# Optimization experiments

Hardware: AMD Instinct MI355X
Metric: run time of the kernel (lower is better)

Reference implementation:

```python
import jax, jax.numpy as jnp
import numpy as np
import math

NUM_HEADS = 16
HIDDEN = 1024
HEAD_DIM = HIDDEN // NUM_HEADS
WIN = 512  # relative position window size
B, S = 2, 2048
LN_EPS = 1e-5


def setup_inputs() -> dict:
    key = jax.random.key(0)
    ks = jax.random.split(key, 8)
    sd = 1.0 / math.sqrt(HIDDEN)
    return {
        "x": jax.random.normal(ks[0], (B, S, HIDDEN), jnp.float32),
        "Wq": jax.random.normal(ks[1], (HIDDEN, HIDDEN), jnp.float32) * sd,
        "bq": jnp.zeros((HIDDEN,), jnp.float32),
        "Wk": jax.random.normal(ks[2], (HIDDEN, HIDDEN), jnp.float32) * sd,
        "bk": jnp.zeros((HIDDEN,), jnp.float32),
        "Wv": jax.random.normal(ks[3], (HIDDEN, HIDDEN), jnp.float32) * sd,
        "bv": jnp.zeros((HIDDEN,), jnp.float32),
        "Wo": jax.random.normal(ks[4], (HIDDEN, HIDDEN), jnp.float32) * sd,
        "bo": jnp.zeros((HIDDEN,), jnp.float32),
        "relpos_table": jax.random.normal(ks[5], (WIN, HIDDEN), jnp.float32),
        "ln_gamma": jnp.ones((HIDDEN,), jnp.float32),
        "ln_beta": jnp.zeros((HIDDEN,), jnp.float32),
        "Wrk": jax.random.normal(ks[6], (HIDDEN, HIDDEN), jnp.float32) * sd,
        "brk": jnp.zeros((HIDDEN,), jnp.float32),
        "Wrq": jax.random.normal(ks[7], (HIDDEN, HIDDEN), jnp.float32) * sd,
        "brq": jnp.zeros((HIDDEN,), jnp.float32),
    }


def reference(x, Wq, bq, Wk, bk, Wv, bv, Wo, bo,
              relpos_table, ln_gamma, ln_beta, Wrk, brk, Wrq, brq):
    Bsz, Slen, H = x.shape
    nh, hd = NUM_HEADS, HEAD_DIM

    # QKV projections -> [B, S, nh, hd]
    q = (x @ Wq + bq).reshape(Bsz, Slen, nh, hd)
    k = (x @ Wk + bk).reshape(Bsz, Slen, nh, hd)
    v = (x @ Wv + bv).reshape(Bsz, Slen, nh, hd)

    mu = relpos_table.mean(-1, keepdims=True)
    var = relpos_table.var(-1, keepdims=True)  # biased, as in torch LayerNorm
    e = (relpos_table - mu) * jax.lax.rsqrt(var + LN_EPS) * ln_gamma + ln_beta

    # relative position index matrix [S, S]: clamp(key - query, -W+1, 0) + W-1
    qi = jnp.arange(Slen)
    relpos = jnp.clip(qi[None, :] - qi[:, None], -WIN + 1, 0) + (WIN - 1)

    rk = (e @ Wrk + brk).reshape(WIN, nh, hd)
    rq = (e @ Wrq + brq).reshape(WIN, nh, hd)

    # content-to-content scores [B, nh, S, S]
    c2c = jnp.einsum('bqhd,bkhd->bhqk', q, k)

    # content-to-position: scores over window then gather along window axis
    qps = jnp.einsum('bnhd,whd->bhnw', q, rk)           # [B, nh, S, W]
    c2p = qps[:, :, qi[:, None], relpos]                # [B, nh, S, S]

    # position-to-content: window x key_seq scores, gather along window axis
    kps = jnp.einsum('bnhd,whd->bhwn', k, rq)           # [B, nh, W, S]
    p2c = kps[:, :, relpos, qi[None, :]]                # [B, nh, S, S]

    scale_factor = 3.0  # 1 + relpos_q_enabled + relpos_k_enabled
    logits = (c2c + c2p + p2c) / math.sqrt(hd * scale_factor)

    # causal mask
    causal = qi[None, :] <= qi[:, None]
    logits = jnp.where(causal[None, None], logits, jnp.finfo(logits.dtype).min)

    attn = jax.nn.softmax(logits, axis=-1)              # [B, nh, S, S]
    out = jnp.einsum('bhqk,bkhd->bqhd', attn, v).reshape(Bsz, Slen, H)
    return out @ Wo + bo
```

## Files before the change

kernel.cpp:

```cpp
#include <hip/hip_runtime.h>
#include <math.h>

#define NH 16
#define HD 64
#define HID 1024
#define SEQ 2048
#define NB 2

typedef __attribute__((ext_vector_type(8))) short short8;
typedef __attribute__((ext_vector_type(4))) float f32x4;
typedef unsigned short u16;
typedef unsigned int u32;

constexpr float LN_EPS_C = 1e-5f;
constexpr float SM_SCALE = 0.07216878364870323f;

__device__ inline u16 f2b(float f) {
  unsigned u = __builtin_bit_cast(unsigned, f);
  u = (u + 0x7FFFu + ((u >> 16) & 1u)) >> 16;
  return (u16)u;
}
__device__ inline float b2f(u16 h) {
  unsigned u = ((unsigned)h) << 16;
  return __builtin_bit_cast(float, u);
}
__device__ inline u32 pk2(float lo, float hi) {
  return (u32)f2b(lo) | ((u32)f2b(hi) << 16);
}
__device__ inline f32x4 mfma16(short8 a, short8 b, f32x4 c) {
  return __builtin_amdgcn_mfma_f32_16x16x32_bf16(a, b, c, 0, 0, 0);
}
__device__ inline short8 swz8(const u16* base, int row, int hc) {
  return *reinterpret_cast<const short8*>(&base[row * 64 + 8 * (hc ^ (row & 7))]);
}
__device__ inline int vrot(int row, int col) {
  return row * 72 + ((col + 16 * ((row >> 3) & 3)) & 63);
}
template <int N>
__device__ inline float rorf(float x) {
  return __builtin_bit_cast(float,
      __builtin_amdgcn_update_dpp(0, __builtin_bit_cast(int, x),
                                  0x120 + N, 0xF, 0xF, true));
}
__device__ inline float rmax16(float x) {
  x = fmaxf(x, rorf<1>(x)); x = fmaxf(x, rorf<2>(x));
  x = fmaxf(x, rorf<4>(x)); x = fmaxf(x, rorf<8>(x));
  return x;
}
__device__ inline float rsum16(float x) {
  x += rorf<1>(x); x += rorf<2>(x); x += rorf<4>(x); x += rorf<8>(x);
  return x;
}

struct PrepArgs {
  const float* tbl; const float* gamma; const float* beta; u16* e;
  const float* x; u16* xb;
  const float* ws[6]; u16* wd[6];
};
__global__ __launch_bounds__(256) void prep_kernel(PrepArgs p) {
  __shared__ float T[32][33];
  __shared__ float sb[4], ssb[4];
  int bid = blockIdx.x;
  int t = threadIdx.x;
  if (bid < 512) {
    int row = bid;
    const float4* rp = reinterpret_cast<const float4*>(p.tbl + (size_t)row * HID);
    float4 x = rp[t];
    float s = x.x + x.y + x.z + x.w;
    float ss = x.x * x.x + x.y * x.y + x.z * x.z + x.w * x.w;
    #pragma unroll
    for (int o = 1; o < 64; o <<= 1) {
      s += __shfl_xor(s, o);
      ss += __shfl_xor(ss, o);
    }
    int w = t >> 6;
    if ((t & 63) == 0) { sb[w] = s; ssb[w] = ss; }
    __syncthreads();
    s = sb[0] + sb[1] + sb[2] + sb[3];
    ss = ssb[0] + ssb[1] + ssb[2] + ssb[3];
    float mu = s * (1.0f / HID);
    float var = ss * (1.0f / HID) - mu * mu;
    float rs = rsqrtf(var + LN_EPS_C);
    float4 g = reinterpret_cast<const float4*>(p.gamma)[t];
    float4 bt = reinterpret_cast<const float4*>(p.beta)[t];
    ushort4 o4;
    o4.x = f2b((x.x - mu) * rs * g.x + bt.x);
    o4.y = f2b((x.y - mu) * rs * g.y + bt.y);
    o4.z = f2b((x.z - mu) * rs * g.z + bt.z);
    o4.w = f2b((x.w - mu) * rs * g.w + bt.w);
    *reinterpret_cast<ushort4*>(&p.e[(size_t)row * HID + t * 4]) = o4;
  } else if (bid < 2560) {
    int i = ((bid - 512) * 256 + t) * 8;
    float4 a = *reinterpret_cast<const float4*>(&p.x[i]);
    float4 c = *reinterpret_cast<const float4*>(&p.x[i + 4]);
    short8 o;
    o[0] = (short)f2b(a.x); o[1] = (short)f2b(a.y); o[2] = (short)f2b(a.z); o[3] = (short)f2b(a.w);
    o[4] = (short)f2b(c.x); o[5] = (short)f2b(c.y); o[6] = (short)f2b(c.z); o[7] = (short)f2b(c.w);
    *reinterpret_cast<short8*>(&p.xb[i]) = o;
  } else {
    int z = (bid - 2560) >> 10;
    int rem = (bid - 2560) & 1023;
    int bn = (rem & 31) * 32, bk = (rem >> 5) * 32;
    const float* W = p.ws[z];
    u16* Wt = p.wd[z];
    int r = t >> 3, c4 = (t & 7) * 4;
    float4 v = *reinterpret_cast<const float4*>(&W[(size_t)(bk + r) * HID + bn + c4]);
    T[r][c4 + 0] = v.x; T[r][c4 + 1] = v.y; T[r][c4 + 2] = v.z; T[r][c4 + 3] = v.w;
    __syncthreads();
    int n = t >> 3, k4 = (t & 7) * 4;
    ushort4 o;
    o.x = f2b(T[k4 + 0][n]); o.y = f2b(T[k4 + 1][n]);
    o.z = f2b(T[k4 + 2][n]); o.w = f2b(T[k4 + 3][n]);
    *reinterpret_cast<ushort4*>(&Wt[(size_t)(bn + n) * HID + bk + k4]) = o;
  }
}

struct GO {
  const float* bias[3];
  void* out[3];
};
template <bool F32OUT>
__global__ __launch_bounds__(512) void gemm_bf16(const u16* __restrict__ A,
    const u16* __restrict__ Bt, GO go) {
  __shared__ u16 Al[8192];
  __shared__ u16 Bl[8192];
  int t = threadIdx.x;
  int gx = gridDim.x;
  int nwg = gx * gridDim.y;
  int lin = blockIdx.y * gx + blockIdx.x;
  lin = (lin & 7) * (nwg >> 3) + (lin >> 3);
  int cb = (lin % gx) * 128, rb = (lin / gx) * 128;
  int which = cb >> 10, cbl = cb & 1023;
  const float* bias = go.bias[which];
  void* Cout = go.out[which];
  int wv = t >> 6, lane = t & 63, l15 = lane & 15, lg = lane >> 4;
  int wr = (wv >> 2) * 64, wc = (wv & 3) * 32;
  int srow = t >> 2, sch = t & 3;
  f32x4 acc[4][2];
  #pragma unroll
  for (int i = 0; i < 4; ++i)
    #pragma unroll
    for (int j = 0; j < 2; ++j) acc[i][j] = (f32x4){0.f, 0.f, 0.f, 0.f};
  const u16* Ap = A + (size_t)(rb + srow) * HID;
  const u16* Bp = Bt + (size_t)(cb + srow) * HID;
  int slot0 = 8 * (sch ^ (srow & 7));
  int slot1 = 8 * ((sch + 4) ^ (srow & 7));
  short8 pa0 = *reinterpret_cast<const short8*>(&Ap[sch * 8]);
  short8 pa1 = *reinterpret_cast<const short8*>(&Ap[(sch + 4) * 8]);
  short8 pb0 = *reinterpret_cast<const short8*>(&Bp[sch * 8]);
  short8 pb1 = *reinterpret_cast<const short8*>(&Bp[(sch + 4) * 8]);
  for (int kk = 0; kk < HID; kk += 64) {
    __syncthreads();
    *reinterpret_cast<short8*>(&Al[srow * 64 + slot0]) = pa0;
    *reinterpret_cast<short8*>(&Al[srow * 64 + slot1]) = pa1;
    *reinterpret_cast<short8*>(&Bl[srow * 64 + slot0]) = pb0;
    *reinterpret_cast<short8*>(&Bl[srow * 64 + slot1]) = pb1;
    __syncthreads();
    if (kk + 64 < HID) {
      pa0 = *reinterpret_cast<const short8*>(&Ap[kk + 64 + sch * 8]);
      pa1 = *reinterpret_cast<const short8*>(&Ap[kk + 64 + (sch + 4) * 8]);
      pb0 = *reinterpret_cast<const short8*>(&Bp[kk + 64 + sch * 8]);
      pb1 = *reinterpret_cast<const short8*>(&Bp[kk + 64 + (sch + 4) * 8]);
    }
    #pragma unroll
    for (int s = 0; s < 2; ++s) {
      short8 am[4], bn[2];
      #pragma unroll
      for (int i = 0; i < 4; ++i) am[i] = swz8(Al, wr + i * 16 + l15, s * 4 + lg);
      #pragma unroll
      for (int j = 0; j < 2; ++j) bn[j] = swz8(Bl, wc + j * 16 + l15, s * 4 + lg);
      #pragma unroll
      for (int i = 0; i < 4; ++i)
        #pragma unroll
        for (int j = 0; j < 2; ++j)
          acc[i][j] = mfma16(am[i], bn[j], acc[i][j]);
    }
  }
  #pragma unroll
  for (int j = 0; j < 2; ++j) {
    float bv = bias[cbl + wc + j * 16 + l15];
    #pragma unroll
    for (int i = 0; i < 4; ++i) {
      #pragma unroll
      for (int r = 0; r < 4; ++r) {
        size_t idx = (size_t)(rb + wr + i * 16 + lg * 4 + r) * HID + cbl + wc + j * 16 + l15;
        float v = acc[i][j][r] + bv;
        if (F32OUT) reinterpret_cast<float*>(Cout)[idx] = v;
        else reinterpret_cast<u16*>(Cout)[idx] = f2b(v);
      }
    }
  }
}

template <bool F32OUT>
__global__ __launch_bounds__(256) void gemm_m64(const u16* __restrict__ A,
    const u16* __restrict__ Bt, GO go) {
  __shared__ u16 Al[4096];
  __shared__ u16 Bl[8192];
  int t = threadIdx.x;
  int gx = gridDim.x;
  int nwg = gx * gridDim.y;
  int lin = blockIdx.y * gx + blockIdx.x;
  lin = (lin & 7) * (nwg >> 3) + (lin >> 3);
  int cb = (lin % gx) * 128, rb = (lin / gx) * 64;
  int which = cb >> 10, cbl = cb & 1023;
  const float* bias = go.bias[which];
  void* Cout = go.out[which];
  int wv = t >> 6, lane = t & 63, l15 = lane & 15, lg = lane >> 4;
  int wc = wv * 32;
  int arow = t >> 2, ach = t & 3;
  int aslot0 = 8 * (ach ^ (arow & 7));
  int aslot1 = 8 * ((ach + 4) ^ (arow & 7));
  int brow = t >> 1, bch = (t & 1) * 4;
  const u16* Ap = A + (size_t)(rb + arow) * HID;
  const u16* Bp = Bt + (size_t)(cb + brow) * HID;
  f32x4 acc[4][2];
  #pragma unroll
  for (int i = 0; i < 4; ++i)
    #pragma unroll
    for (int j = 0; j < 2; ++j) acc[i][j] = (f32x4){0.f, 0.f, 0.f, 0.f};
  short8 pa0 = *reinterpret_cast<const short8*>(&Ap[ach * 8]);
  short8 pa1 = *reinterpret_cast<const short8*>(&Ap[(ach + 4) * 8]);
  short8 pb[4];
  #pragma unroll
  for (int j = 0; j < 4; ++j)
    pb[j] = *reinterpret_cast<const short8*>(&Bp[(bch + j) * 8]);
  for (int kk = 0; kk < HID; kk += 64) {
    __syncthreads();
    *reinterpret_cast<short8*>(&Al[arow * 64 + aslot0]) = pa0;
    *reinterpret_cast<short8*>(&Al[arow * 64 + aslot1]) = pa1;
    #pragma unroll
    for (int j = 0; j < 4; ++j)
      *reinterpret_cast<short8*>(&Bl[brow * 64 + 8 * ((bch + j) ^ (brow & 7))]) = pb[j];
    __syncthreads();
    if (kk + 64 < HID) {
      pa0 = *reinterpret_cast<const short8*>(&Ap[kk + 64 + ach * 8]);
      pa1 = *reinterpret_cast<const short8*>(&Ap[kk + 64 + (ach + 4) * 8]);
      #pragma unroll
      for (int j = 0; j < 4; ++j)
        pb[j] = *reinterpret_cast<const short8*>(&Bp[kk + 64 + (bch + j) * 8]);
    }
    #pragma unroll
    for (int s = 0; s < 2; ++s) {
      short8 am[4], bn[2];
      #pragma unroll
      for (int i = 0; i < 4; ++i) am[i] = swz8(Al, i * 16 + l15, s * 4 + lg);
      #pragma unroll
      for (int j = 0; j < 2; ++j) bn[j] = swz8(Bl, wc + j * 16 + l15, s * 4 + lg);
      #pragma unroll
      for (int i = 0; i < 4; ++i)
        #pragma unroll
        for (int j = 0; j < 2; ++j)
          acc[i][j] = mfma16(am[i], bn[j], acc[i][j]);
    }
  }
  #pragma unroll
  for (int j = 0; j < 2; ++j) {
    float bv = bias[cbl + wc + j * 16 + l15];
    #pragma unroll
    for (int i = 0; i < 4; ++i) {
      #pragma unroll
      for (int r = 0; r < 4; ++r) {
        size_t idx = (size_t)(rb + i * 16 + lg * 4 + r) * HID + cbl + wc + j * 16 + l15;
        float v = acc[i][j][r] + bv;
        if (F32OUT) reinterpret_cast<float*>(Cout)[idx] = v;
        else reinterpret_cast<u16*>(Cout)[idx] = f2b(v);
      }
    }
  }
}

__global__ __launch_bounds__(256, 3) void bias_kernel(
    const u16* __restrict__ Qb, const u16* __restrict__ Kb,
    const u16* __restrict__ RKb, const u16* __restrict__ RQb,
    u16* __restrict__ bandT, float* __restrict__ qrk0,
    float* __restrict__ krq0) {
  __shared__ u16 smem[20992];
  const int KsO = 0, UO = 4096;
  const int RKO = UO, RQO = UO + 8192;
  const int G1O = UO, G2O = UO + 8448;

  int qt = blockIdx.x;
  int h = blockIdx.y, b = blockIdx.z;
  int q0 = qt * 64;
  int t = threadIdx.x;
  int wv = t >> 6, lane = t & 63, l15 = lane & 15, lg = lane >> 4;
  int qs = q0 + wv * 16;
  int hoff = h * HD;
  int bh = (b * NH + h) * SEQ;

  {
    int i = q0 + (t >> 2);
    int sub = t & 3;
    size_t rbase = (size_t)(b * SEQ + i) * HID + hoff + sub * 16;
    size_t tb2 = (size_t)hoff + sub * 16;
    float s1 = 0.f, s2 = 0.f;
    #pragma unroll
    for (int c = 0; c < 2; ++c) {
      short8 qv = *reinterpret_cast<const short8*>(&Qb[rbase + c * 8]);
      short8 rv = *reinterpret_cast<const short8*>(&RKb[tb2 + c * 8]);
      short8 kv = *reinterpret_cast<const short8*>(&Kb[rbase + c * 8]);
      short8 uv = *reinterpret_cast<const short8*>(&RQb[tb2 + c * 8]);
      #pragma unroll
      for (int j = 0; j < 8; ++j) {
        s1 += b2f((u16)qv[j]) * b2f((u16)rv[j]);
        s2 += b2f((u16)kv[j]) * b2f((u16)uv[j]);
      }
    }
    s1 += __shfl_xor(s1, 1); s1 += __shfl_xor(s1, 2);
    s2 += __shfl_xor(s2, 1); s2 += __shfl_xor(s2, 2);
    if (sub == 0) { qrk0[bh + i] = s1 * SM_SCALE; krq0[bh + i] = s2 * SM_SCALE; }
  }

  size_t qgrow = (size_t)(b * SEQ + qs + l15) * HID + hoff;
  short8 aq0 = *reinterpret_cast<const short8*>(&Qb[qgrow + lg * 8]);
  short8 aq1 = *reinterpret_cast<const short8*>(&Qb[qgrow + 32 + lg * 8]);

  const f32x4 Z = (f32x4){0.f, 0.f, 0.f, 0.f};
  int vr = t >> 2, vc8 = (t & 3) * 8;
  int ktlo = qt - 8; if (ktlo < 0) ktlo = 0;
  size_t tbase = (((size_t)(b * NH + h) * 32 + qt) * 9) << 12;

  for (int kt = ktlo; kt <= qt; ++kt) {
    int k0 = kt * 64;
    int dt = qt - kt;
    int wlo = 448 - 64 * dt; if (wlo < 0) wlo = 0;
    __syncthreads();
    {
      const u16* kg = &Kb[(size_t)(b * SEQ + k0 + vr) * HID + hoff];
      int c0 = vc8 >> 3;
      *reinterpret_cast<short8*>(&smem[KsO + vr * 64 + 8 * (c0 ^ (vr & 7))]) =
          *reinterpret_cast<const short8*>(&kg[vc8]);
      *reinterpret_cast<short8*>(&smem[KsO + vr * 64 + 8 * ((c0 + 4) ^ (vr & 7))]) =
          *reinterpret_cast<const short8*>(&kg[vc8 + 32]);
    }
    for (int e2 = t; e2 < 1024; e2 += 256) {
      int rr = e2 >> 3, cch = e2 & 7;
      int wr2 = wlo + rr; if (wr2 > 511) wr2 = 511;
      size_t gb = (size_t)wr2 * HID + hoff + cch * 8;
      int slot = 8 * (cch ^ (rr & 7));
      *reinterpret_cast<short8*>(&smem[RKO + rr * 64 + slot]) =
          *reinterpret_cast<const short8*>(&RKb[gb]);
      *reinterpret_cast<short8*>(&smem[RQO + rr * 64 + slot]) =
          *reinterpret_cast<const short8*>(&RQb[gb]);
    }
    __syncthreads();
    u32 g1p[16], g2p[16];
    #pragma unroll
    for (int cw = 0; cw < 8; ++cw) {
      short8 r0 = swz8(&smem[RKO], cw * 16 + l15, lg);
      short8 r1 = swz8(&smem[RKO], cw * 16 + l15, 4 + lg);
      f32x4 g = mfma16(r1, aq1, mfma16(r0, aq0, Z));
      g1p[2 * cw] = pk2(g[0], g[1]);
      g1p[2 * cw + 1] = pk2(g[2], g[3]);
    }
    short8 kw0 = swz8(&smem[KsO], wv * 16 + l15, lg);
    short8 kw1 = swz8(&smem[KsO], wv * 16 + l15, 4 + lg);
    #pragma unroll
    for (int cw = 0; cw < 8; ++cw) {
      short8 u0 = swz8(&smem[RQO], cw * 16 + l15, lg);
      short8 u1 = swz8(&smem[RQO], cw * 16 + l15, 4 + lg);
      f32x4 g = mfma16(u1, kw1, mfma16(u0, kw0, Z));
      g2p[2 * cw] = pk2(g[0], g[1]);
      g2p[2 * cw + 1] = pk2(g[2], g[3]);
    }
    __syncthreads();
    #pragma unroll
    for (int cw = 0; cw < 8; ++cw) {
      *reinterpret_cast<uint2*>(&smem[G1O + (wv * 16 + l15) * 132 + cw * 16 + lg * 4]) =
          make_uint2(g1p[2 * cw], g1p[2 * cw + 1]);
      *reinterpret_cast<uint2*>(&smem[G2O + (wv * 16 + l15) * 132 + cw * 16 + lg * 4]) =
          make_uint2(g2p[2 * cw], g2p[2 * cw + 1]);
    }
    __syncthreads();
    u16* outp = bandT + tbase + ((size_t)dt << 12) + t * 16;
    #pragma unroll
    for (int c = 0; c < 4; ++c) {
      float vv[4];
      #pragma unroll
      for (int r = 0; r < 4; ++r) {
        int q = qs + lg * 4 + r;
        int k = k0 + c * 16 + l15;
        int wi = 511 - (q - k) - wlo; if (wi < 0) wi = 0;
        vv[r] = (b2f(smem[G1O + (wv * 16 + lg * 4 + r) * 132 + wi]) +
                 b2f(smem[G2O + (c * 16 + l15) * 132 + wi])) * SM_SCALE;
      }
      *reinterpret_cast<uint2*>(outp + c * 4) =
          make_uint2(pk2(vv[0], vv[1]), pk2(vv[2], vv[3]));
    }
  }
}

__global__ __launch_bounds__(256, 2) void attn_mfma(
    const u16* __restrict__ Qb, const u16* __restrict__ Kb,
    const u16* __restrict__ Vb, const float* __restrict__ qrk0,
    const float* __restrict__ krq0, const u16* __restrict__ bandT,
    u16* __restrict__ ATT) {
  __shared__ u16 smem[22016];
  const int KsB[2] = {0, 4096};
  const int VtB[2] = {8192, 12800};
  const int PsO = 17408;

  int qtA = 31 - (int)blockIdx.x;
  int qtB = (int)blockIdx.x;
  int h = blockIdx.y, b = blockIdx.z;
  int t = threadIdx.x;
  int wv = t >> 6, lane = t & 63, l15 = lane & 15, lg = lane >> 4;
  int hoff = h * HD;
  int bh = (b * NH + h) * SEQ;
  size_t tbaseA = (((size_t)(b * NH + h) * 32 + qtA) * 9) << 12;
  size_t tbaseB = (((size_t)(b * NH + h) * 32 + qtB) * 9) << 12;

  int qsA = qtA * 64 + wv * 16;
  int qsB = qtB * 64 + wv * 16;
  size_t qgA = (size_t)(b * SEQ + qsA + l15) * HID + hoff;
  size_t qgB = (size_t)(b * SEQ + qsB + l15) * HID + hoff;
  short8 aqA0 = *reinterpret_cast<const short8*>(&Qb[qgA + lg * 8]);
  short8 aqA1 = *reinterpret_cast<const short8*>(&Qb[qgA + 32 + lg * 8]);
  short8 aqB0 = *reinterpret_cast<const short8*>(&Qb[qgB + lg * 8]);
  short8 aqB1 = *reinterpret_cast<const short8*>(&Qb[qgB + 32 + lg * 8]);
  float qb0A[4], qb0B[4];
  #pragma unroll
  for (int r = 0; r < 4; ++r) {
    qb0A[r] = qrk0[bh + qsA + lg * 4 + r];
    qb0B[r] = qrk0[bh + qsB + lg * 4 + r];
  }

  float mA[4], lA[4], mB[4], lB[4];
  f32x4 oA[4], oB[4];
  #pragma unroll
  for (int r = 0; r < 4; ++r) { mA[r] = -INFINITY; lA[r] = 0.f; mB[r] = -INFINITY; lB[r] = 0.f; }
  #pragma unroll
  for (int c = 0; c < 4; ++c) {
    oA[c] = (f32x4){0.f, 0.f, 0.f, 0.f};
    oB[c] = (f32x4){0.f, 0.f, 0.f, 0.f};
  }

  const f32x4 Z = (f32x4){0.f, 0.f, 0.f, 0.f};
  int vr = t >> 2, vc8 = (t & 3) * 8;
  int c0s = vc8 >> 3;
  int kslot0 = vr * 64 + 8 * (c0s ^ (vr & 7));
  int kslot1 = vr * 64 + 8 * ((c0s + 4) ^ (vr & 7));
  int vslot[16];
  #pragma unroll
  for (int j = 0; j < 8; ++j) {
    vslot[j] = vrot(vc8 + j, vr);
    vslot[8 + j] = vrot(vc8 + 32 + j, vr);
  }

  {
    const u16* kg = &Kb[(size_t)(b * SEQ + vr) * HID + hoff];
    short8 k0v = *reinterpret_cast<const short8*>(&kg[vc8]);
    short8 k1v = *reinterpret_cast<const short8*>(&kg[vc8 + 32]);
    *reinterpret_cast<short8*>(&smem[KsB[0] + kslot0]) = k0v;
    *reinterpret_cast<short8*>(&smem[KsB[0] + kslot1]) = k1v;
    const u16* vg = &Vb[(size_t)(b * SEQ + vr) * HID + hoff];
    short8 v0v = *reinterpret_cast<const short8*>(&vg[vc8]);
    short8 v1v = *reinterpret_cast<const short8*>(&vg[vc8 + 32]);
    #pragma unroll
    for (int j = 0; j < 8; ++j) smem[VtB[0] + vslot[j]] = (u16)v0v[j];
    #pragma unroll
    for (int j = 0; j < 8; ++j) smem[VtB[0] + vslot[8 + j]] = (u16)v1v[j];
  }
  __syncthreads();

  int cur = 0;
  for (int kt = 0; kt <= qtA; ++kt) {
    int k0 = kt * 64;
    int dtA = qtA - kt;
    bool doB = (kt <= qtB);
    int dtB = qtB - kt;
    bool bandedA = (dtA <= 8);
    bool bandedB = doB && (dtB <= 8);
    int ksb = KsB[cur], vtb = VtB[cur];
    int ksn = KsB[cur ^ 1], vtn = VtB[cur ^ 1];

    short8 pA0, pA1, pB0, pB1;
    if (bandedA) {
      const u16* tb = bandT + tbaseA + ((size_t)dtA << 12) + t * 16;
      pA0 = *reinterpret_cast<const short8*>(tb);
      pA1 = *reinterpret_cast<const short8*>(tb + 8);
    }
    if (bandedB) {
      const u16* tb = bandT + tbaseB + ((size_t)dtB << 12) + t * 16;
      pB0 = *reinterpret_cast<const short8*>(tb);
      pB1 = *reinterpret_cast<const short8*>(tb + 8);
    }
    float kq[4];
    if (dtA > 8 || (doB && dtB > 8)) {
      #pragma unroll
      for (int c = 0; c < 4; ++c) kq[c] = krq0[bh + k0 + c * 16 + l15];
    }
    short8 nk0, nk1, nv0, nv1;
    if (kt < qtA) {
      const u16* kg = &Kb[(size_t)(b * SEQ + k0 + 64 + vr) * HID + hoff];
      nk0 = *reinterpret_cast<const short8*>(&kg[vc8]);
      nk1 = *reinterpret_cast<const short8*>(&kg[vc8 + 32]);
      const u16* vg = &Vb[(size_t)(b * SEQ + k0 + 64 + vr) * HID + hoff];
      nv0 = *reinterpret_cast<const short8*>(&vg[vc8]);
      nv1 = *reinterpret_cast<const short8*>(&vg[vc8 + 32]);
    }

    short8 kb0[4], kb1[4];
    #pragma unroll
    for (int c = 0; c < 4; ++c) {
      kb0[c] = swz8(&smem[ksb], c * 16 + l15, lg);
      kb1[c] = swz8(&smem[ksb], c * 16 + l15, 4 + lg);
    }
    f32x4 sA[4], sB[4];
    __builtin_amdgcn_s_setprio(1);
    #pragma unroll
    for (int c = 0; c < 4; ++c)
      sA[c] = mfma16(aqA1, kb1[c], mfma16(aqA0, kb0[c], Z));
    if (doB) {
      #pragma unroll
      for (int c = 0; c < 4; ++c)
        sB[c] = mfma16(aqB1, kb1[c], mfma16(aqB0, kb0[c], Z));
    }
    __builtin_amdgcn_s_setprio(0);
    #pragma unroll
    for (int c = 0; c < 4; ++c) {
      #pragma unroll
      for (int r = 0; r < 4; ++r) {
        float bbv = bandedA ? b2f((u16)((c < 2 ? pA0 : pA1)[(c & 1) * 4 + r]))
                            : qb0A[r] + kq[c];
        float v = fmaf(sA[c][r], SM_SCALE, bbv);
        if (dtA == 0) {
          int ql = wv * 16 + lg * 4 + r, kl = c * 16 + l15;
          if (ql < kl) v = -INFINITY;
        }
        sA[c][r] = v;
      }
    }
    if (doB) {
      #pragma unroll
      for (int c = 0; c < 4; ++c) {
        #pragma unroll
        for (int r = 0; r < 4; ++r) {
          float bbv = bandedB ? b2f((u16)((c < 2 ? pB0 : pB1)[(c & 1) * 4 + r]))
                              : qb0B[r] + kq[c];
          float v = fmaf(sB[c][r], SM_SCALE, bbv);
          if (dtB == 0) {
            int ql = wv * 16 + lg * 4 + r, kl = c * 16 + l15;
            if (ql < kl) v = -INFINITY;
          }
          sB[c][r] = v;
        }
      }
    }
    float alA[4], alB[4];
    #pragma unroll
    for (int r = 0; r < 4; ++r) {
      float mx = fmaxf(fmaxf(sA[0][r], sA[1][r]), fmaxf(sA[2][r], sA[3][r]));
      mx = rmax16(mx);
      float mn = fmaxf(mA[r], mx);
      alA[r] = __expf(mA[r] - mn);
      float ps = 0.f;
      #pragma unroll
      for (int c = 0; c < 4; ++c) {
        float p = __expf(sA[c][r] - mn);
        sA[c][r] = p;
        ps += p;
      }
      ps = rsum16(ps);
      lA[r] = lA[r] * alA[r] + ps;
      mA[r] = mn;
    }
    if (doB) {
      #pragma unroll
      for (int r = 0; r < 4; ++r) {
        float mx = fmaxf(fmaxf(sB[0][r], sB[1][r]), fmaxf(sB[2][r], sB[3][r]));
        mx = rmax16(mx);
        float mn = fmaxf(mB[r], mx);
        alB[r] = __expf(mB[r] - mn);
        float ps = 0.f;
        #pragma unroll
        for (int c = 0; c < 4; ++c) {
          float p = __expf(sB[c][r] - mn);
          sB[c][r] = p;
          ps += p;
        }
        ps = rsum16(ps);
        lB[r] = lB[r] * alB[r] + ps;
        mB[r] = mn;
      }
    }
    short8 vb0[4], vb1[4];
    #pragma unroll
    for (int c = 0; c < 4; ++c) {
      int n = c * 16 + l15;
      vb0[c] = *reinterpret_cast<const short8*>(&smem[vtb + vrot(n, lg * 8)]);
      vb1[c] = *reinterpret_cast<const short8*>(&smem[vtb + vrot(n, 32 + lg * 8)]);
    }
    #pragma unroll
    for (int c = 0; c < 4; ++c) {
      #pragma unroll
      for (int r = 0; r < 4; ++r) {
        smem[PsO + vrot(wv * 16 + lg * 4 + r, c * 16 + l15)] = f2b(sA[c][r]);
        oA[c][r] *= alA[r];
      }
    }
    int prow = wv * 16 + l15;
    {
      short8 ap0 = *reinterpret_cast<const short8*>(&smem[PsO + vrot(prow, lg * 8)]);
      short8 ap1 = *reinterpret_cast<const short8*>(&smem[PsO + vrot(prow, 32 + lg * 8)]);
      __builtin_amdgcn_s_setprio(1);
      #pragma unroll
      for (int c = 0; c < 4; ++c)
        oA[c] = mfma16(ap1, vb1[c], mfma16(ap0, vb0[c], oA[c]));
      __builtin_amdgcn_s_setprio(0);
    }
    if (doB) {
      #pragma unroll
      for (int c = 0; c < 4; ++c) {
        #pragma unroll
        for (int r = 0; r < 4; ++r) {
          smem[PsO + vrot(wv * 16 + lg * 4 + r, c * 16 + l15)] = f2b(sB[c][r]);
          oB[c][r] *= alB[r];
        }
      }
      short8 bp0 = *reinterpret_cast<const short8*>(&smem[PsO + vrot(prow, lg * 8)]);
      short8 bp1 = *reinterpret_cast<const short8*>(&smem[PsO + vrot(prow, 32 + lg * 8)]);
      __builtin_amdgcn_s_setprio(1);
      #pragma unroll
      for (int c = 0; c < 4; ++c)
        oB[c] = mfma16(bp1, vb1[c], mfma16(bp0, vb0[c], oB[c]));
      __builtin_amdgcn_s_setprio(0);
    }
    if (kt < qtA) {
      *reinterpret_cast<short8*>(&smem[ksn + kslot0]) = nk0;
      *reinterpret_cast<short8*>(&smem[ksn + kslot1]) = nk1;
      #pragma unroll
      for (int j = 0; j < 8; ++j) smem[vtn + vslot[j]] = (u16)nv0[j];
      #pragma unroll
      for (int j = 0; j < 8; ++j) smem[vtn + vslot[8 + j]] = (u16)nv1[j];
    }
    __syncthreads();
    cur ^= 1;
  }
  #pragma unroll
  for (int r = 0; r < 4; ++r) { lA[r] = 1.0f / lA[r]; lB[r] = 1.0f / lB[r]; }
  #pragma unroll
  for (int c = 0; c < 4; ++c) {
    #pragma unroll
    for (int r = 0; r < 4; ++r) {
      size_t obA = (size_t)(b * SEQ + qsA + lg * 4 + r) * HID + hoff + c * 16 + l15;
      ATT[obA] = f2b(oA[c][r] * lA[r]);
      size_t obB = (size_t)(b * SEQ + qsB + lg * 4 + r) * HID + hoff + c * 16 + l15;
      ATT[obB] = f2b(oB[c][r] * lB[r]);
    }
  }
}

extern "C" void kernel_launch(void* const* d_in, const int* in_sizes, int n_in,
                              void* d_out, int out_size, void* d_ws, size_t ws_size,
                              hipStream_t stream) {
  const float* x      = (const float*)d_in[0];
  const float* Wq     = (const float*)d_in[1];
  const float* bq     = (const float*)d_in[2];
  const float* Wk     = (const float*)d_in[3];
  const float* bk     = (const float*)d_in[4];
  const float* Wv     = (const float*)d_in[5];
  const float* bv     = (const float*)d_in[6];
  const float* Wo     = (const float*)d_in[7];
  const float* bo     = (const float*)d_in[8];
  const float* relpos = (const float*)d_in[9];
  const float* gamma  = (const float*)d_in[10];
  const float* beta   = (const float*)d_in[11];
  const float* Wrk    = (const float*)d_in[12];
  const float* brk    = (const float*)d_in[13];
  const float* Wrq    = (const float*)d_in[14];
  const float* brq    = (const float*)d_in[15];
  float* out = (float*)d_out;

  u16* wsu = (u16*)d_ws;
  size_t off = 0;
  auto alloc = [&](size_t n) { u16* p = wsu + off; off += n; return p; };
  u16* xb   = alloc(4194304);
  u16* Eb   = alloc(524288);
  u16* WtQ  = alloc(1048576);
  u16* WtK  = alloc(1048576);
  u16* WtV  = alloc(1048576);
  u16* WtO  = alloc(1048576);
  u16* WtRK = alloc(1048576);
  u16* WtRQ = alloc(1048576);
  u16* Qb2  = alloc(4194304);
  u16* Kb2  = alloc(4194304);
  u16* Vb2  = alloc(4194304);
  u16* ATTb = alloc(4194304);
  u16* RKb2 = alloc(524288);
  u16* RQb2 = alloc(524288);
  float* qrk0 = (float*)(wsu + off); off += 131072;
  float* krq0 = (float*)(wsu + off); off += 131072;
  u16* bandT = alloc((size_t)NB * NH * 32 * 9 * 4096);

  PrepArgs pa;
  pa.tbl = relpos; pa.gamma = gamma; pa.beta = beta; pa.e = Eb;
  pa.x = x; pa.xb = xb;
  pa.ws[0] = Wq; pa.ws[1] = Wk; pa.ws[2] = Wv; pa.ws[3] = Wo; pa.ws[4] = Wrk; pa.ws[5] = Wrq;
  pa.wd[0] = WtQ; pa.wd[1] = WtK; pa.wd[2] = WtV; pa.wd[3] = WtO; pa.wd[4] = WtRK; pa.wd[5] = WtRQ;
  prep_kernel<<<8704, 256, 0, stream>>>(pa);

  GO goQKV = {{bq, bk, bv}, {Qb2, Kb2, Vb2}};
  dim3 gQKV(24, 32);
  gemm_bf16<false><<<gQKV, 512, 0, stream>>>(xb, WtQ, goQKV);
  GO goRel = {{brk, brq, brq}, {RKb2, RQb2, RQb2}};
  dim3 gRel2(16, 8);
  gemm_m64<false><<<gRel2, 256, 0, stream>>>(Eb, WtRK, goRel);

  dim3 gB(32, NH, NB);
  bias_kernel<<<gB, 256, 0, stream>>>(Qb2, Kb2, RKb2, RQb2, bandT, qrk0, krq0);

  dim3 gA(16, NH, NB);
  attn_mfma<<<gA, 256, 0, stream>>>(Qb2, Kb2, Vb2, qrk0, krq0, bandT, ATTb);

  GO goOut = {{bo, bo, bo}, {out, out, out}};
  dim3 gOut(8, 64);
  gemm_m64<true><<<gOut, 256, 0, stream>>>(ATTb, WtO, goOut);
}
```

Baseline: 210.7 us.

## Merge QKV and relpos GEMMs into one launch, use exp2 softmax, remap attention blocks

Folds the relative-position projection GEMM into the QKV GEMM launch as extra 128x128 tiles, which removes one kernel launch and lets the small GEMM share the machine with the large one. Moves the log2(e) factor into the softmax scale and the precomputed bias terms so the softmax can use the raw v_exp_f32 instruction instead of __expf. Remaps attention block indices with a stride-8 interleave, which changes how blocks are spread across compute units. The exp2 path depends on every bias source being scaled consistently, and the relpos tiles now run with the 512-thread 128-row tiling.

Measured after the change: 200.2 us. 5.0% less time.

```diff
diff --git a/kernel.cpp b/kernel.cpp
--- a/kernel.cpp
+++ b/kernel.cpp
@@ -14,6 +14,7 @@
 
 constexpr float LN_EPS_C = 1e-5f;
 constexpr float SM_SCALE = 0.07216878364870323f;
+constexpr float SM_SCALE2 = 0.07216878364870323f * 1.4426950408889634f;
 
 __device__ inline u16 f2b(float f) {
   unsigned u = __builtin_bit_cast(unsigned, f);
@@ -29,6 +30,11 @@
 }
 __device__ inline f32x4 mfma16(short8 a, short8 b, f32x4 c) {
   return __builtin_amdgcn_mfma_f32_16x16x32_bf16(a, b, c, 0, 0, 0);
+}
+__device__ inline float ex2(float x) {
+  float r;
+  asm("v_exp_f32 %0, %1" : "=v"(r) : "v"(x));
+  return r;
 }
 __device__ inline short8 swz8(const u16* base, int row, int hc) {
   return *reinterpret_cast<const short8*>(&base[row * 64 + 8 * (hc ^ (row & 7))]);
@@ -115,24 +121,33 @@
   }
 }
 
-struct GO {
-  const float* bias[3];
-  void* out[3];
+struct G5 {
+  const float* bias[5];
+  u16* out[5];
 };
-template <bool F32OUT>
-__global__ __launch_bounds__(512) void gemm_bf16(const u16* __restrict__ A,
-    const u16* __restrict__ Bt, GO go) {
+__global__ __launch_bounds__(512) void gemm_qkvrel(const u16* __restrict__ xb,
+    const u16* __restrict__ WtQKV, const u16* __restrict__ Eb,
+    const u16* __restrict__ WtRel, G5 g5) {
   __shared__ u16 Al[8192];
   __shared__ u16 Bl[8192];
   int t = threadIdx.x;
-  int gx = gridDim.x;
-  int nwg = gx * gridDim.y;
-  int lin = blockIdx.y * gx + blockIdx.x;
-  lin = (lin & 7) * (nwg >> 3) + (lin >> 3);
-  int cb = (lin % gx) * 128, rb = (lin / gx) * 128;
-  int which = cb >> 10, cbl = cb & 1023;
-  const float* bias = go.bias[which];
-  void* Cout = go.out[which];
+  int raw = blockIdx.x;
+  int lin = (raw & 7) * 104 + (raw >> 3);
+  const u16 *A, *Bt;
+  const float* bias;
+  u16* Cout;
+  int rb, cb;
+  if (lin < 768) {
+    cb = (lin % 24) * 128; rb = (lin / 24) * 128;
+    A = xb; Bt = WtQKV;
+    bias = g5.bias[cb >> 10]; Cout = g5.out[cb >> 10];
+  } else {
+    int j = lin - 768;
+    cb = (j & 15) * 128; rb = (j >> 4) * 128;
+    A = Eb; Bt = WtRel;
+    bias = g5.bias[3 + (cb >> 10)]; Cout = g5.out[3 + (cb >> 10)];
+  }
+  int cbl = cb & 1023;
   int wv = t >> 6, lane = t & 63, l15 = lane & 15, lg = lane >> 4;
   int wr = (wv >> 2) * 64, wc = (wv & 3) * 32;
   int srow = t >> 2, sch = t & 3;
@@ -184,15 +199,16 @@
       #pragma unroll
       for (int r = 0; r < 4; ++r) {
         size_t idx = (size_t)(rb + wr + i * 16 + lg * 4 + r) * HID + cbl + wc + j * 16 + l15;
-        float v = acc[i][j][r] + bv;
-        if (F32OUT) reinterpret_cast<float*>(Cout)[idx] = v;
-        else reinterpret_cast<u16*>(Cout)[idx] = f2b(v);
-      }
-    }
-  }
-}
-
-template <bool F32OUT>
+        Cout[idx] = f2b(acc[i][j][r] + bv);
+      }
+    }
+  }
+}
+
+struct GO {
+  const float* bias;
+  float* out;
+};
 __global__ __launch_bounds__(256) void gemm_m64(const u16* __restrict__ A,
     const u16* __restrict__ Bt, GO go) {
   __shared__ u16 Al[4096];
@@ -203,9 +219,8 @@
   int lin = blockIdx.y * gx + blockIdx.x;
   lin = (lin & 7) * (nwg >> 3) + (lin >> 3);
   int cb = (lin % gx) * 128, rb = (lin / gx) * 64;
-  int which = cb >> 10, cbl = cb & 1023;
-  const float* bias = go.bias[which];
-  void* Cout = go.out[which];
+  const float* bias = go.bias;
+  float* Cout = go.out;
   int wv = t >> 6, lane = t & 63, l15 = lane & 15, lg = lane >> 4;
   int wc = wv * 32;
   int arow = t >> 2, ach = t & 3;
@@ -256,15 +271,13 @@
   }
   #pragma unroll
   for (int j = 0; j < 2; ++j) {
-    float bv = bias[cbl + wc + j * 16 + l15];
+    float bv = bias[cb + wc + j * 16 + l15];
     #pragma unroll
     for (int i = 0; i < 4; ++i) {
       #pragma unroll
       for (int r = 0; r < 4; ++r) {
-        size_t idx = (size_t)(rb + i * 16 + lg * 4 + r) * HID + cbl + wc + j * 16 + l15;
-        float v = acc[i][j][r] + bv;
-        if (F32OUT) reinterpret_cast<float*>(Cout)[idx] = v;
-        else reinterpret_cast<u16*>(Cout)[idx] = f2b(v);
+        size_t idx = (size_t)(rb + i * 16 + lg * 4 + r) * HID + cb + wc + j * 16 + l15;
+        Cout[idx] = acc[i][j][r] + bv;
       }
     }
   }
@@ -309,7 +322,7 @@
     }
     s1 += __shfl_xor(s1, 1); s1 += __shfl_xor(s1, 2);
     s2 += __shfl_xor(s2, 1); s2 += __shfl_xor(s2, 2);
-    if (sub == 0) { qrk0[bh + i] = s1 * SM_SCALE; krq0[bh + i] = s2 * SM_SCALE; }
+    if (sub == 0) { qrk0[bh + i] = s1 * SM_SCALE2; krq0[bh + i] = s2 * SM_SCALE2; }
   }
 
   size_t qgrow = (size_t)(b * SEQ + qs + l15) * HID + hoff;
@@ -383,7 +396,7 @@
         int k = k0 + c * 16 + l15;
         int wi = 511 - (q - k) - wlo; if (wi < 0) wi = 0;
         vv[r] = (b2f(smem[G1O + (wv * 16 + lg * 4 + r) * 132 + wi]) +
-                 b2f(smem[G2O + (c * 16 + l15) * 132 + wi])) * SM_SCALE;
+                 b2f(smem[G2O + (c * 16 + l15) * 132 + wi])) * SM_SCALE2;
       }
       *reinterpret_cast<uint2*>(outp + c * 4) =
           make_uint2(pk2(vv[0], vv[1]), pk2(vv[2], vv[3]));
@@ -401,9 +414,13 @@
   const int VtB[2] = {8192, 12800};
   const int PsO = 17408;
 
-  int qtA = 31 - (int)blockIdx.x;
-  int qtB = (int)blockIdx.x;
-  int h = blockIdx.y, b = blockIdx.z;
+  int flat = (int)blockIdx.x + 16 * ((int)blockIdx.y + 16 * (int)blockIdx.z);
+  flat = (flat & 7) * 64 + (flat >> 3);
+  int pairi = flat & 15;
+  int h = (flat >> 4) & 15;
+  int b = flat >> 8;
+  int qtA = 31 - pairi;
+  int qtB = pairi;
   int t = threadIdx.x;
   int wv = t >> 6, lane = t & 63, l15 = lane & 15, lg = lane >> 4;
   int hoff = h * HD;
@@ -524,7 +541,7 @@
       for (int r = 0; r < 4; ++r) {
         float bbv = bandedA ? b2f((u16)((c < 2 ? pA0 : pA1)[(c & 1) * 4 + r]))
                             : qb0A[r] + kq[c];
-        float v = fmaf(sA[c][r], SM_SCALE, bbv);
+        float v = fmaf(sA[c][r], SM_SCALE2, bbv);
         if (dtA == 0) {
           int ql = wv * 16 + lg * 4 + r, kl = c * 16 + l15;
           if (ql < kl) v = -INFINITY;
@@ -539,7 +556,7 @@
         for (int r = 0; r < 4; ++r) {
           float bbv = bandedB ? b2f((u16)((c < 2 ? pB0 : pB1)[(c & 1) * 4 + r]))
                               : qb0B[r] + kq[c];
-          float v = fmaf(sB[c][r], SM_SCALE, bbv);
+          float v = fmaf(sB[c][r], SM_SCALE2, bbv);
           if (dtB == 0) {
             int ql = wv * 16 + lg * 4 + r, kl = c * 16 + l15;
             if (ql < kl) v = -INFINITY;
@@ -554,11 +571,11 @@
       float mx = fmaxf(fmaxf(sA[0][r], sA[1][r]), fmaxf(sA[2][r], sA[3][r]));
       mx = rmax16(mx);
       float mn = fmaxf(mA[r], mx);
-      alA[r] = __expf(mA[r] - mn);
+      alA[r] = ex2(mA[r] - mn);
       float ps = 0.f;
       #pragma unroll
       for (int c = 0; c < 4; ++c) {
-        float p = __expf(sA[c][r] - mn);
+        float p = ex2(sA[c][r] - mn);
         sA[c][r] = p;
         ps += p;
       }
@@ -572,11 +589,11 @@
         float mx = fmaxf(fmaxf(sB[0][r], sB[1][r]), fmaxf(sB[2][r], sB[3][r]));
         mx = rmax16(mx);
         float mn = fmaxf(mB[r], mx);
-        alB[r] = __expf(mB[r] - mn);
+        alB[r] = ex2(mB[r] - mn);
         float ps = 0.f;
         #pragma unroll
         for (int c = 0; c < 4; ++c) {
-          float p = __expf(sB[c][r] - mn);
+          float p = ex2(sB[c][r] - mn);
           sB[c][r] = p;
           ps += p;
         }
@@ -701,12 +718,10 @@
   pa.wd[0] = WtQ; pa.wd[1] = WtK; pa.wd[2] = WtV; pa.wd[3] = WtO; pa.wd[4] = WtRK; pa.wd[5] = WtRQ;
   prep_kernel<<<8704, 256, 0, stream>>>(pa);
 
-  GO goQKV = {{bq, bk, bv}, {Qb2, Kb2, Vb2}};
-  dim3 gQKV(24, 32);
-  gemm_bf16<false><<<gQKV, 512, 0, stream>>>(xb, WtQ, goQKV);
-  GO goRel = {{brk, brq, brq}, {RKb2, RQb2, RQb2}};
-  dim3 gRel2(16, 8);
-  gemm_m64<false><<<gRel2, 256, 0, stream>>>(Eb, WtRK, goRel);
+  G5 g5;
+  g5.bias[0] = bq; g5.bias[1] = bk; g5.bias[2] = bv; g5.bias[3] = brk; g5.bias[4] = brq;
+  g5.out[0] = Qb2; g5.out[1] = Kb2; g5.out[2] = Vb2; g5.out[3] = RKb2; g5.out[4] = RQb2;
+  gemm_qkvrel<<<832, 512, 0, stream>>>(xb, WtQ, Eb, WtRK, g5);
 
   dim3 gB(32, NH, NB);
   bias_kernel<<<gB, 256, 0, stream>>>(Qb2, Kb2, RKb2, RQb2, bandT, qrk0, krq0);
@@ -714,7 +729,7 @@
   dim3 gA(16, NH, NB);
   attn_mfma<<<gA, 256, 0, stream>>>(Qb2, Kb2, Vb2, qrk0, krq0, bandT, ATTb);
 
-  GO goOut = {{bo, bo, bo}, {out, out, out}};
+  GO goOut = {bo, out};
   dim3 gOut(8, 64);
-  gemm_m64<true><<<gOut, 256, 0, stream>>>(ATTb, WtO, goOut);
-}
+  gemm_m64<<<gOut, 256, 0, stream>>>(ATTb, WtO, goOut);
+}
```
